# Kernel optimization log

Measured on AMD Instinct MI355X. Metric: run time of the kernel, lower is better.

Reference implementation:

```python
import jax, jax.numpy as jnp
import numpy as np

B, T, N_EMBD, N_HEAD = 2, 2048, 1024, 16
HEAD = N_EMBD // N_HEAD
WINDOW = 64


def setup_inputs() -> dict:
    key = jax.random.key(0)
    kq, kk, kv, kw = jax.random.split(key, 4)
    q = jax.random.normal(kq, (B, T, N_EMBD), dtype=jnp.float32)
    k = jax.random.normal(kk, (B, T, N_EMBD), dtype=jnp.float32)
    v = jax.random.normal(kv, (B, T, N_EMBD), dtype=jnp.float32)
    W_proj = jax.random.normal(kw, (N_EMBD, N_EMBD), dtype=jnp.float32) * (1.0 / np.sqrt(N_EMBD))
    b_proj = jnp.zeros((N_EMBD,), dtype=jnp.float32)
    return {"q": q, "k": k, "v": v, "W_proj": W_proj, "b_proj": b_proj}


def reference(q, k, v, W_proj, b_proj):
    Bsz, Tlen, _ = q.shape
    # split heads: [B, H, T, D]
    qh = q.reshape(Bsz, Tlen, N_HEAD, HEAD).transpose(0, 2, 1, 3)
    kh = k.reshape(Bsz, Tlen, N_HEAD, HEAD).transpose(0, 2, 1, 3)
    vh = v.reshape(Bsz, Tlen, N_HEAD, HEAD).transpose(0, 2, 1, 3)

    scale = 1.0 / np.sqrt(HEAD)
    scores = jnp.einsum('bhqd,bhkd->bhqk', qh, kh) * scale  # [B,H,T,T]

    # windowed additive mask: positions with |i-j| > WINDOW get -inf
    idx = jnp.arange(Tlen)
    dist = jnp.abs(idx[None, :] - idx[:, None])  # [T, T]
    scores = jnp.where(dist[None, None] > WINDOW, -jnp.inf, scores)

    attn = jax.nn.softmax(scores, axis=-1)
    y = jnp.einsum('bhqk,bhkd->bhqd', attn, vh)  # [B,H,T,D]
    y = y.transpose(0, 2, 1, 3).reshape(Bsz, Tlen, N_EMBD)
    return y @ W_proj.T + b_proj
```

## Files before the change

kernel.cpp:

```cpp
#include <hip/hip_runtime.h>
#include <hip/hip_bf16.h>

#define B_SZ 2
#define T_SZ 2048
#define NE   1024
#define NH   16
#define HD   64
#define WIN  64
#define QT   64
#define KT   192
#define GM   4096
#define GN   1024
#define GK   1024
#define KPAD 72
#define VPAD 200

__device__ ushort Wb_static[GN * GK];

__device__ __forceinline__ ushort f2bf(float x) {
    union { float f; uint u; } a; a.f = x;
    uint r = (a.u + 0x7fffu + ((a.u >> 16) & 1u)) >> 16;
    return (ushort)r;
}
__device__ __forceinline__ uint pack2(float a, float b) {
    return (uint)f2bf(a) | ((uint)f2bf(b) << 16);
}
__device__ __forceinline__ uint4 pack8(float4 a, float4 b) {
    return make_uint4(pack2(a.x, a.y), pack2(a.z, a.w),
                      pack2(b.x, b.y), pack2(b.z, b.w));
}

typedef __attribute__((ext_vector_type(8))) short frag_ab;
typedef __attribute__((ext_vector_type(4))) float frag_cd;

__global__ __launch_bounds__(256) void attn_mfma_kernel(
    const float* __restrict__ q, const float* __restrict__ k,
    const float* __restrict__ v, const float* __restrict__ W,
    ushort* __restrict__ y)
{
    __shared__ __attribute__((aligned(16))) ushort pool[KT * KPAD + HD * VPAD];
    ushort* Ks = pool;
    ushort* Vt = pool + KT * KPAD;
    ushort* Ps = pool;

    const int qs = blockIdx.x * QT;
    const int h  = blockIdx.y;
    const int b  = blockIdx.z;
    const int t  = threadIdx.x;
    const int kstart = qs - WIN;

    {
        const int bid = blockIdx.x + 32 * blockIdx.y + 512 * blockIdx.z;
        const int idx = bid * 256 + t;
        const float4 f = ((const float4*)W)[idx];
        ((uint2*)Wb_static)[idx] = make_uint2(pack2(f.x, f.y), pack2(f.z, f.w));
    }

    for (int c = t; c < KT * 8; c += 256) {
        const int j  = c >> 3;
        const int cc = c & 7;
        const int d8 = cc * 8;
        const int jg = kstart + j;
        float4 k0 = make_float4(0,0,0,0), k1 = make_float4(0,0,0,0);
        float4 v0 = make_float4(0,0,0,0), v1 = make_float4(0,0,0,0);
        if (jg >= 0 && jg < T_SZ) {
            const size_t off = ((size_t)(b * T_SZ + jg)) * NE + h * HD + d8;
            const float4* kp = (const float4*)(k + off);
            const float4* vp = (const float4*)(v + off);
            k0 = kp[0]; k1 = kp[1];
            v0 = vp[0]; v1 = vp[1];
        }
        *(uint4*)&Ks[j * KPAD + d8] = pack8(k0, k1);
        ushort* vtc = &Vt[d8 * VPAD + (((j >> 3) ^ cc) * 8 + (j & 7))];
        vtc[0 * VPAD] = f2bf(v0.x); vtc[1 * VPAD] = f2bf(v0.y);
        vtc[2 * VPAD] = f2bf(v0.z); vtc[3 * VPAD] = f2bf(v0.w);
        vtc[4 * VPAD] = f2bf(v1.x); vtc[5 * VPAD] = f2bf(v1.y);
        vtc[6 * VPAD] = f2bf(v1.z); vtc[7 * VPAD] = f2bf(v1.w);
    }

    const int wv   = t >> 6;
    const int L    = t & 63;
    const int r16  = L & 15;
    const int quad = L >> 4;

    frag_ab aq0, aq1;
    {
        const float* qrow = q + ((size_t)(b * T_SZ + qs + wv * 16 + r16)) * NE + h * HD;
        const float4* p0 = (const float4*)(qrow + quad * 8);
        const float4* p1 = (const float4*)(qrow + 32 + quad * 8);
        float4 f0 = p0[0], f1 = p0[1], g0 = p1[0], g1 = p1[1];
        aq0[0] = (short)f2bf(f0.x * 0.125f); aq0[1] = (short)f2bf(f0.y * 0.125f);
        aq0[2] = (short)f2bf(f0.z * 0.125f); aq0[3] = (short)f2bf(f0.w * 0.125f);
        aq0[4] = (short)f2bf(f1.x * 0.125f); aq0[5] = (short)f2bf(f1.y * 0.125f);
        aq0[6] = (short)f2bf(f1.z * 0.125f); aq0[7] = (short)f2bf(f1.w * 0.125f);
        aq1[0] = (short)f2bf(g0.x * 0.125f); aq1[1] = (short)f2bf(g0.y * 0.125f);
        aq1[2] = (short)f2bf(g0.z * 0.125f); aq1[3] = (short)f2bf(g0.w * 0.125f);
        aq1[4] = (short)f2bf(g1.x * 0.125f); aq1[5] = (short)f2bf(g1.y * 0.125f);
        aq1[6] = (short)f2bf(g1.z * 0.125f); aq1[7] = (short)f2bf(g1.w * 0.125f);
    }
    __syncthreads();

    frag_cd sacc[12];
#pragma unroll
    for (int nb = 0; nb < 12; ++nb) sacc[nb] = (frag_cd){0,0,0,0};
#pragma unroll
    for (int nb = 0; nb < 12; ++nb) {
        const frag_ab b0 = *(const frag_ab*)&Ks[(nb * 16 + r16) * KPAD + quad * 8];
        const frag_ab b1 = *(const frag_ab*)&Ks[(nb * 16 + r16) * KPAD + 32 + quad * 8];
        sacc[nb] = __builtin_amdgcn_mfma_f32_16x16x32_bf16(aq0, b0, sacc[nb], 0, 0, 0);
        sacc[nb] = __builtin_amdgcn_mfma_f32_16x16x32_bf16(aq1, b1, sacc[nb], 0, 0, 0);
    }

    const int base_m = wv * 16 + quad * 4;
    float l[4] = {0.f, 0.f, 0.f, 0.f};
#pragma unroll
    for (int nb = 0; nb < 12; ++nb) {
        const int jl = nb * 16 + r16;
        const int jg = kstart + jl;
        const bool jg_ok = (jg >= 0) & (jg < T_SZ);
#pragma unroll
        for (int r = 0; r < 4; ++r) {
            const int mrow = base_m + r;
            const bool valid = jg_ok & (jl >= mrow) & (jl <= mrow + 2 * WIN);
            const float p = valid ? __expf(sacc[nb][r]) : 0.0f;
            l[r] += p;
            sacc[nb][r] = p;
        }
    }
#pragma unroll
    for (int r = 0; r < 4; ++r) {
        l[r] += __shfl_xor(l[r], 1);
        l[r] += __shfl_xor(l[r], 2);
        l[r] += __shfl_xor(l[r], 4);
        l[r] += __shfl_xor(l[r], 8);
    }

    __syncthreads();
#pragma unroll
    for (int nb = 0; nb < 12; ++nb) {
        const int jl = nb * 16 + r16;
#pragma unroll
        for (int r = 0; r < 4; ++r)
            Ps[(base_m + r) * VPAD + jl] = f2bf(sacc[nb][r]);
    }
    __syncthreads();

    frag_ab ap[6];
#pragma unroll
    for (int kb = 0; kb < 6; ++kb)
        ap[kb] = *(const frag_ab*)&Ps[(wv * 16 + r16) * VPAD + kb * 32 + quad * 8];

    frag_cd oacc[4];
#pragma unroll
    for (int nb = 0; nb < 4; ++nb) oacc[nb] = (frag_cd){0,0,0,0};
#pragma unroll
    for (int nb = 0; nb < 4; ++nb) {
        const int dr  = nb * 16 + r16;
        const int dsw = (dr >> 3) & 7;
#pragma unroll
        for (int kb = 0; kb < 6; ++kb) {
            const frag_ab bv = *(const frag_ab*)&Vt[dr * VPAD + (((kb * 4 + quad) ^ dsw) * 8)];
            oacc[nb] = __builtin_amdgcn_mfma_f32_16x16x32_bf16(ap[kb], bv, oacc[nb], 0, 0, 0);
        }
    }

    float inv[4];
#pragma unroll
    for (int r = 0; r < 4; ++r) inv[r] = 1.0f / l[r];
#pragma unroll
    for (int nb = 0; nb < 4; ++nb) {
#pragma unroll
        for (int r = 0; r < 4; ++r) {
            const int iq = qs + base_m + r;
            const int d  = nb * 16 + r16;
            y[((size_t)(b * T_SZ + iq)) * NE + h * HD + d] = f2bf(oacc[nb][r] * inv[r]);
        }
    }
}

__global__ __launch_bounds__(256) void proj_gemm_kernel(
    const ushort* __restrict__ A,
    const float* __restrict__ bias, float* __restrict__ C)
{
    __shared__ __attribute__((aligned(16))) ushort As[128 * 64];
    __shared__ __attribute__((aligned(16))) ushort Bs[64 * 64];

    const ushort* Bw = Wb_static;
    const int t      = threadIdx.x;
    const int tile_n = blockIdx.x;
    const int tile_m = blockIdx.y;
    const int lane   = t & 63;
    const int wv     = t >> 6;
    const int wm     = wv >> 1;
    const int wn     = wv & 1;
    const int r16    = lane & 15;
    const int quad   = lane >> 4;

    frag_cd acc[4][2];
#pragma unroll
    for (int mi = 0; mi < 4; ++mi)
#pragma unroll
        for (int ni = 0; ni < 2; ++ni)
            acc[mi][ni] = (frag_cd){0.0f, 0.0f, 0.0f, 0.0f};

    const int fm  = wm * 64 + r16;
    const int fn  = wn * 32 + r16;
    const int sw  = r16 & 7;
    const int ca0 = (quad ^ sw) * 8;
    const int ca1 = ((4 + quad) ^ sw) * 8;

    for (int k0 = 0; k0 < GK; k0 += 64) {
#pragma unroll
        for (int i = 0; i < 4; ++i) {
            const int c   = t + 256 * i;
            const int row = c >> 3;
            const int src = ((c & 7) ^ (row & 7)) * 8;
            __builtin_amdgcn_global_load_lds(
                (const __attribute__((address_space(1))) unsigned int*)
                    (A + (size_t)(tile_m * 128 + row) * GK + k0 + src),
                (__attribute__((address_space(3))) unsigned int*)(As + c * 8), 16, 0, 0);
        }
#pragma unroll
        for (int i = 0; i < 2; ++i) {
            const int c   = t + 256 * i;
            const int row = c >> 3;
            const int src = ((c & 7) ^ (row & 7)) * 8;
            __builtin_amdgcn_global_load_lds(
                (const __attribute__((address_space(1))) unsigned int*)
                    (Bw + (size_t)(tile_n * 64 + row) * GK + k0 + src),
                (__attribute__((address_space(3))) unsigned int*)(Bs + c * 8), 16, 0, 0);
        }
        __syncthreads();

        frag_ab a0[4], a1[4], b0[2], b1[2];
#pragma unroll
        for (int mi = 0; mi < 4; ++mi) {
            a0[mi] = *(const frag_ab*)&As[(fm + mi * 16) * 64 + ca0];
            a1[mi] = *(const frag_ab*)&As[(fm + mi * 16) * 64 + ca1];
        }
#pragma unroll
        for (int ni = 0; ni < 2; ++ni) {
            b0[ni] = *(const frag_ab*)&Bs[(fn + ni * 16) * 64 + ca0];
            b1[ni] = *(const frag_ab*)&Bs[(fn + ni * 16) * 64 + ca1];
        }

#pragma unroll
        for (int mi = 0; mi < 4; ++mi)
#pragma unroll
            for (int ni = 0; ni < 2; ++ni) {
                acc[mi][ni] = __builtin_amdgcn_mfma_f32_16x16x32_bf16(
                    a0[mi], b0[ni], acc[mi][ni], 0, 0, 0);
                acc[mi][ni] = __builtin_amdgcn_mfma_f32_16x16x32_bf16(
                    a1[mi], b1[ni], acc[mi][ni], 0, 0, 0);
            }

        __syncthreads();
    }

#pragma unroll
    for (int mi = 0; mi < 4; ++mi) {
#pragma unroll
        for (int ni = 0; ni < 2; ++ni) {
            const int rbase = tile_m * 128 + wm * 64 + mi * 16 + quad * 4;
            const int cg    = tile_n * 64 + wn * 32 + ni * 16 + r16;
            const float bv  = bias[cg];
#pragma unroll
            for (int r = 0; r < 4; ++r)
                C[(size_t)(rbase + r) * GN + cg] = acc[mi][ni][r] + bv;
        }
    }
}

extern "C" void kernel_launch(void* const* d_in, const int* in_sizes, int n_in,
                              void* d_out, int out_size, void* d_ws, size_t ws_size,
                              hipStream_t stream) {
    (void)in_sizes; (void)n_in; (void)out_size; (void)ws_size;
    const float* q    = (const float*)d_in[0];
    const float* k    = (const float*)d_in[1];
    const float* v    = (const float*)d_in[2];
    const float* W    = (const float*)d_in[3];
    const float* bias = (const float*)d_in[4];
    float*  out = (float*)d_out;
    ushort* y   = (ushort*)d_ws;

    dim3 g1(T_SZ / QT, NH, B_SZ);
    attn_mfma_kernel<<<g1, 256, 0, stream>>>(q, k, v, W, y);

    dim3 g2(GN / 64, GM / 128);
    proj_gemm_kernel<<<g2, 256, 0, stream>>>(y, bias, out);
}
```

Measured before the change: 128.2 us.

## Swizzle block order, deepen GEMM K tile, clamp K/V loads, raise MFMA priority

Both kernels now use a 1D grid with an XCD-aware block swizzle so that neighbouring tiles land on the same chiplet and share cache. The projection GEMM doubles its K tile to 128 per stage, which halves the number of barrier-separated iterations at the cost of twice the LDS per block. The attention K/V staging loop is fully unrolled and replaces the bounds branch with clamped indices; out-of-range rows are still masked later during softmax. s_setprio is raised around the MFMA sections to favour the matrix work when waves are scheduled.

```diff
diff --git a/kernel.cpp b/kernel.cpp
--- a/kernel.cpp
+++ b/kernel.cpp
@@ -43,33 +43,33 @@
     ushort* Vt = pool + KT * KPAD;
     ushort* Ps = pool;
 
-    const int qs = blockIdx.x * QT;
-    const int h  = blockIdx.y;
-    const int b  = blockIdx.z;
-    const int t  = threadIdx.x;
+    const int bid = blockIdx.x;
+    const int swz = ((bid & 7) << 7) | (bid >> 3);
+    const int qs  = (swz & 31) * QT;
+    const int h   = (swz >> 5) & 15;
+    const int b   = swz >> 9;
+    const int t   = threadIdx.x;
     const int kstart = qs - WIN;
 
     {
-        const int bid = blockIdx.x + 32 * blockIdx.y + 512 * blockIdx.z;
         const int idx = bid * 256 + t;
         const float4 f = ((const float4*)W)[idx];
         ((uint2*)Wb_static)[idx] = make_uint2(pack2(f.x, f.y), pack2(f.z, f.w));
     }
 
-    for (int c = t; c < KT * 8; c += 256) {
+#pragma unroll
+    for (int i = 0; i < 6; ++i) {
+        const int c  = t + 256 * i;
         const int j  = c >> 3;
         const int cc = c & 7;
         const int d8 = cc * 8;
         const int jg = kstart + j;
-        float4 k0 = make_float4(0,0,0,0), k1 = make_float4(0,0,0,0);
-        float4 v0 = make_float4(0,0,0,0), v1 = make_float4(0,0,0,0);
-        if (jg >= 0 && jg < T_SZ) {
-            const size_t off = ((size_t)(b * T_SZ + jg)) * NE + h * HD + d8;
-            const float4* kp = (const float4*)(k + off);
-            const float4* vp = (const float4*)(v + off);
-            k0 = kp[0]; k1 = kp[1];
-            v0 = vp[0]; v1 = vp[1];
-        }
+        const int jc = min(max(jg, 0), T_SZ - 1);
+        const size_t off = ((size_t)(b * T_SZ + jc)) * NE + h * HD + d8;
+        const float4* kp = (const float4*)(k + off);
+        const float4* vp = (const float4*)(v + off);
+        const float4 k0 = kp[0], k1 = kp[1];
+        const float4 v0 = vp[0], v1 = vp[1];
         *(uint4*)&Ks[j * KPAD + d8] = pack8(k0, k1);
         ushort* vtc = &Vt[d8 * VPAD + (((j >> 3) ^ cc) * 8 + (j & 7))];
         vtc[0 * VPAD] = f2bf(v0.x); vtc[1 * VPAD] = f2bf(v0.y);
@@ -103,6 +103,7 @@
     frag_cd sacc[12];
 #pragma unroll
     for (int nb = 0; nb < 12; ++nb) sacc[nb] = (frag_cd){0,0,0,0};
+    __builtin_amdgcn_s_setprio(1);
 #pragma unroll
     for (int nb = 0; nb < 12; ++nb) {
         const frag_ab b0 = *(const frag_ab*)&Ks[(nb * 16 + r16) * KPAD + quad * 8];
@@ -110,6 +111,7 @@
         sacc[nb] = __builtin_amdgcn_mfma_f32_16x16x32_bf16(aq0, b0, sacc[nb], 0, 0, 0);
         sacc[nb] = __builtin_amdgcn_mfma_f32_16x16x32_bf16(aq1, b1, sacc[nb], 0, 0, 0);
     }
+    __builtin_amdgcn_s_setprio(0);
 
     const int base_m = wv * 16 + quad * 4;
     float l[4] = {0.f, 0.f, 0.f, 0.f};
@@ -153,6 +155,7 @@
     frag_cd oacc[4];
 #pragma unroll
     for (int nb = 0; nb < 4; ++nb) oacc[nb] = (frag_cd){0,0,0,0};
+    __builtin_amdgcn_s_setprio(1);
 #pragma unroll
     for (int nb = 0; nb < 4; ++nb) {
         const int dr  = nb * 16 + r16;
@@ -163,6 +166,7 @@
             oacc[nb] = __builtin_amdgcn_mfma_f32_16x16x32_bf16(ap[kb], bv, oacc[nb], 0, 0, 0);
         }
     }
+    __builtin_amdgcn_s_setprio(0);
 
     float inv[4];
 #pragma unroll
@@ -182,13 +186,15 @@
     const ushort* __restrict__ A,
     const float* __restrict__ bias, float* __restrict__ C)
 {
-    __shared__ __attribute__((aligned(16))) ushort As[128 * 64];
-    __shared__ __attribute__((aligned(16))) ushort Bs[64 * 64];
+    __shared__ __attribute__((aligned(16))) ushort As[128 * 128];
+    __shared__ __attribute__((aligned(16))) ushort Bs[64 * 128];
 
     const ushort* Bw = Wb_static;
-    const int t      = threadIdx.x;
-    const int tile_n = blockIdx.x;
-    const int tile_m = blockIdx.y;
+    const int t   = threadIdx.x;
+    const int bid = blockIdx.x;
+    const int swz = ((bid & 7) << 6) | (bid >> 3);
+    const int tile_n = swz & 15;
+    const int tile_m = swz >> 4;
     const int lane   = t & 63;
     const int wv     = t >> 6;
     const int wm     = wv >> 1;
@@ -203,28 +209,26 @@
         for (int ni = 0; ni < 2; ++ni)
             acc[mi][ni] = (frag_cd){0.0f, 0.0f, 0.0f, 0.0f};
 
-    const int fm  = wm * 64 + r16;
-    const int fn  = wn * 32 + r16;
-    const int sw  = r16 & 7;
-    const int ca0 = (quad ^ sw) * 8;
-    const int ca1 = ((4 + quad) ^ sw) * 8;
-
-    for (int k0 = 0; k0 < GK; k0 += 64) {
-#pragma unroll
-        for (int i = 0; i < 4; ++i) {
+    const int fm = wm * 64 + r16;
+    const int fn = wn * 32 + r16;
+    const int sw = r16 & 7;
+
+    for (int k0 = 0; k0 < GK; k0 += 128) {
+#pragma unroll
+        for (int i = 0; i < 8; ++i) {
             const int c   = t + 256 * i;
-            const int row = c >> 3;
-            const int src = ((c & 7) ^ (row & 7)) * 8;
+            const int row = c >> 4;
+            const int src = ((c & 15) ^ (row & 7)) * 8;
             __builtin_amdgcn_global_load_lds(
                 (const __attribute__((address_space(1))) unsigned int*)
                     (A + (size_t)(tile_m * 128 + row) * GK + k0 + src),
                 (__attribute__((address_space(3))) unsigned int*)(As + c * 8), 16, 0, 0);
         }
 #pragma unroll
-        for (int i = 0; i < 2; ++i) {
+        for (int i = 0; i < 4; ++i) {
             const int c   = t + 256 * i;
-            const int row = c >> 3;
-            const int src = ((c & 7) ^ (row & 7)) * 8;
+            const int row = c >> 4;
+            const int src = ((c & 15) ^ (row & 7)) * 8;
             __builtin_amdgcn_global_load_lds(
                 (const __attribute__((address_space(1))) unsigned int*)
                     (Bw + (size_t)(tile_n * 64 + row) * GK + k0 + src),
@@ -232,27 +236,23 @@
         }
         __syncthreads();
 
-        frag_ab a0[4], a1[4], b0[2], b1[2];
-#pragma unroll
-        for (int mi = 0; mi < 4; ++mi) {
-            a0[mi] = *(const frag_ab*)&As[(fm + mi * 16) * 64 + ca0];
-            a1[mi] = *(const frag_ab*)&As[(fm + mi * 16) * 64 + ca1];
-        }
-#pragma unroll
-        for (int ni = 0; ni < 2; ++ni) {
-            b0[ni] = *(const frag_ab*)&Bs[(fn + ni * 16) * 64 + ca0];
-            b1[ni] = *(const frag_ab*)&Bs[(fn + ni * 16) * 64 + ca1];
-        }
-
-#pragma unroll
-        for (int mi = 0; mi < 4; ++mi)
-#pragma unroll
-            for (int ni = 0; ni < 2; ++ni) {
-                acc[mi][ni] = __builtin_amdgcn_mfma_f32_16x16x32_bf16(
-                    a0[mi], b0[ni], acc[mi][ni], 0, 0, 0);
-                acc[mi][ni] = __builtin_amdgcn_mfma_f32_16x16x32_bf16(
-                    a1[mi], b1[ni], acc[mi][ni], 0, 0, 0);
-            }
+#pragma unroll
+        for (int ks = 0; ks < 4; ++ks) {
+            const int cidx = (((ks * 4) + quad) ^ sw) * 8;
+            frag_ab af[4], bfr[2];
+#pragma unroll
+            for (int mi = 0; mi < 4; ++mi)
+                af[mi] = *(const frag_ab*)&As[(fm + mi * 16) * 128 + cidx];
+#pragma unroll
+            for (int ni = 0; ni < 2; ++ni)
+                bfr[ni] = *(const frag_ab*)&Bs[(fn + ni * 16) * 128 + cidx];
+#pragma unroll
+            for (int mi = 0; mi < 4; ++mi)
+#pragma unroll
+                for (int ni = 0; ni < 2; ++ni)
+                    acc[mi][ni] = __builtin_amdgcn_mfma_f32_16x16x32_bf16(
+                        af[mi], bfr[ni], acc[mi][ni], 0, 0, 0);
+        }
 
         __syncthreads();
     }
@@ -283,9 +283,9 @@
     float*  out = (float*)d_out;
     ushort* y   = (ushort*)d_ws;
 
-    dim3 g1(T_SZ / QT, NH, B_SZ);
+    dim3 g1(1024);
     attn_mfma_kernel<<<g1, 256, 0, stream>>>(q, k, v, W, y);
 
-    dim3 g2(GN / 64, GM / 128);
+    dim3 g2(512);
     proj_gemm_kernel<<<g2, 256, 0, stream>>>(y, bias, out);
 }
```

After: 121.2 us. -5.5%, faster.
